# Optimization experiments

Measured on AMD Instinct MI355X. Metric: run time of the kernel, lower is better.

Reference implementation:

```python
import jax, jax.numpy as jnp
import numpy as np

INF = 10000.0

# ---------- differentiable (jax) pieces ----------

def _embed(x, W1, b1, W2, b2):
    # nn.Sequential(Linear, Dropout(eval=identity), ReLU, Linear, ReLU)
    h = jax.nn.relu(x @ W1.T + b1)
    return jax.nn.relu(h @ W2.T + b2)


def _cdist(a, b):
    # batched euclidean cdist with zero-safe sqrt (matches torch.cdist values)
    sq = (jnp.sum(a * a, -1)[:, :, None]
          + jnp.sum(b * b, -1)[:, None, :]
          - 2.0 * jnp.einsum('bnd,bmd->bnm', a, b))
    sq = jnp.maximum(sq, 0.0)
    safe = jnp.where(sq > 0, sq, 1.0)
    return jnp.where(sq > 0, jnp.sqrt(safe), 0.0)


def _edit_costs(x_s, x_t, W1, b1, W2, b2, virtual, B, N):
    D = W2.shape[0]
    es = _embed(x_s, W1, b1, W2, b2).reshape(B, N, D)
    et = _embed(x_t, W1, b1, W2, b2).reshape(B, N, D)
    v = _embed(virtual[None, :], W1, b1, W2, b2)          # [1, D]
    vb = jnp.broadcast_to(v[None, :, :], (B, 1, D))
    es = jnp.concatenate([es, vb], axis=1)                # [B, N+1, D]
    et = jnp.concatenate([et, vb], axis=1)
    d = _cdist(es, et)                                    # [B, N+1, N+1]
    # per-pair normalization: d / sum(d) * (len_s * len_t)
    d = d / jnp.sum(d, axis=(1, 2), keepdims=True) * float(N * N)
    return d

# ---------- host-side LSAPE (replaces scipy.optimize.linear_sum_assignment) ----------

def _lsap(C):
    # Jonker-Volgenant / shortest augmenting path, square cost matrix.
    n = C.shape[0]
    u = np.zeros(n + 1)
    v = np.zeros(n + 1)
    p = np.zeros(n + 1, np.int64)    # p[j] = row matched to column j (1-indexed)
    way = np.zeros(n + 1, np.int64)
    for i in range(1, n + 1):
        p[0] = i
        j0 = 0
        minv = np.full(n + 1, np.inf)
        used = np.zeros(n + 1, bool)
        while True:
            used[j0] = True
            i0 = p[j0]
            free = np.nonzero(~used)[0]
            cur = C[i0 - 1, free - 1] - u[i0] - v[free]
            better = cur < minv[free]
            minv[free] = np.where(better, cur, minv[free])
            way[free] = np.where(better, j0, way[free])
            k = int(np.argmin(minv[free]))
            j1 = int(free[k])
            delta = minv[free][k]
            u[p[used]] += delta
            v[used] -= delta
            minv[free] -= delta
            j0 = j1
            if p[j0] == 0:
                break
        while j0 != 0:
            j1 = int(way[j0])
            p[j0] = p[j1]
            j0 = j1
    rows = p[1:] - 1
    cols = np.arange(n)
    return rows, cols


def _lsape(ec, n, m):
    # ec: (n+1, m+1) edit costs with virtual row/col; build (n+m)x(n+m) LSAPE matrix
    C = np.zeros((n + m, n + m))
    C[:n, :m] = ec[:n, :m]
    C[n:, :m] = INF
    C[:n, m:] = INF
    C[np.arange(n, n + m), np.arange(m)] = ec[n, :m]       # insertions
    C[np.arange(n), np.arange(m, m + n)] = ec[:n, m]       # deletions
    C[~np.isfinite(C)] = INF
    q, p = _lsap(C)
    A = np.zeros((n + 1, m + 1), np.int64)
    A[np.minimum(q, n), np.minimum(p, m)] = 1
    A[-1, -1] = 0
    return A

# ---------- harness ----------

def setup_inputs() -> dict:
    B, N, FIN, D = 16, 128, 512, 512
    key = jax.random.key(0)
    ks = jax.random.split(key, 7)
    s1 = 1.0 / np.sqrt(FIN)
    s2 = 1.0 / np.sqrt(D)
    return {
        'x_s': jax.random.normal(ks[0], (B * N, FIN), jnp.float32),
        'x_t': jax.random.normal(ks[1], (B * N, FIN), jnp.float32),
        'W1': jax.random.uniform(ks[2], (D, FIN), jnp.float32, -s1, s1),
        'b1': jax.random.uniform(ks[3], (D,), jnp.float32, -s1, s1),
        'W2': jax.random.uniform(ks[4], (D, D), jnp.float32, -s2, s2),
        'b2': jax.random.uniform(ks[5], (D,), jnp.float32, -s2, s2),
        'virtual': jax.random.uniform(ks[6], (FIN,), jnp.float32),
        'npairs': 16,
        'n_nodes': 128,
    }


def reference(x_s, x_t, W1, b1, W2, b2, virtual, npairs, n_nodes):
    B, N = int(npairs), int(n_nodes)
    edit = _edit_costs(x_s, x_t, W1, b1, W2, b2, virtual, B, N)  # [B, N+1, N+1]
    ec_np = np.asarray(jax.device_get(edit), np.float64)
    aligns = np.stack([_lsape(ec_np[i], N, N) for i in range(B)])
    A = jnp.asarray(aligns)                                      # [B, N+1, N+1] int
    geds = jnp.sum(A * edit, axis=(1, 2)) / float(2 * N)         # / (len_s + len_t)
    return (A, edit, geds)
```

## Files before the change

### kernel.cpp

```cpp
#include <hip/hip_runtime.h>

#define BATCH 16
#define NNODE 128
#define DIM 512
#define NP1 129
#define EDSZ (NP1 * NP1)
#define BIGF 3.0e38f

__global__ __launch_bounds__(256) void gemm2_nt_relu(
    const float* __restrict__ X0, const float* __restrict__ X1,
    const float* __restrict__ VS,
    const float* __restrict__ W, const float* __restrict__ bias,
    float* __restrict__ Y0, float* __restrict__ Y1,
    int M, int N, int K) {
  if (blockIdx.x == gridDim.x - 1 && blockIdx.z) return;
  const float* X = blockIdx.z ? X1 : X0;
  float* Y = blockIdx.z ? Y1 : Y0;
  __shared__ float sA[32][68];
  __shared__ float sB[32][68];
  const int tid = threadIdx.x;
  const int m0 = blockIdx.x * 64;
  const int n0 = blockIdx.y * 64;
  const int tm = tid / 16, tn = tid % 16;
  const int lr = tid >> 2;
  const int lk8 = (tid & 3) * 8;
  const int row = m0 + lr;
  const float* xrow = (row < M) ? (X + (size_t)row * K) : VS;
  const float* wrow = W + (size_t)(n0 + lr) * K;
  float acc[4][4] = {};
  for (int k0 = 0; k0 < K; k0 += 32) {
    const float* xa = xrow + k0 + lk8;
    const float* wb = wrow + k0 + lk8;
    float4 a0 = *(const float4*)(xa);
    float4 a1 = *(const float4*)(xa + 4);
    float4 b0 = *(const float4*)(wb);
    float4 b1 = *(const float4*)(wb + 4);
    sA[lk8 + 0][lr] = a0.x; sA[lk8 + 1][lr] = a0.y;
    sA[lk8 + 2][lr] = a0.z; sA[lk8 + 3][lr] = a0.w;
    sA[lk8 + 4][lr] = a1.x; sA[lk8 + 5][lr] = a1.y;
    sA[lk8 + 6][lr] = a1.z; sA[lk8 + 7][lr] = a1.w;
    sB[lk8 + 0][lr] = b0.x; sB[lk8 + 1][lr] = b0.y;
    sB[lk8 + 2][lr] = b0.z; sB[lk8 + 3][lr] = b0.w;
    sB[lk8 + 4][lr] = b1.x; sB[lk8 + 5][lr] = b1.y;
    sB[lk8 + 6][lr] = b1.z; sB[lk8 + 7][lr] = b1.w;
    __syncthreads();
#pragma unroll
    for (int k = 0; k < 32; ++k) {
      const float4 a = *(const float4*)&sA[k][tm * 4];
      const float4 b = *(const float4*)&sB[k][tn * 4];
      acc[0][0] = fmaf(a.x, b.x, acc[0][0]);
      acc[0][1] = fmaf(a.x, b.y, acc[0][1]);
      acc[0][2] = fmaf(a.x, b.z, acc[0][2]);
      acc[0][3] = fmaf(a.x, b.w, acc[0][3]);
      acc[1][0] = fmaf(a.y, b.x, acc[1][0]);
      acc[1][1] = fmaf(a.y, b.y, acc[1][1]);
      acc[1][2] = fmaf(a.y, b.z, acc[1][2]);
      acc[1][3] = fmaf(a.y, b.w, acc[1][3]);
      acc[2][0] = fmaf(a.z, b.x, acc[2][0]);
      acc[2][1] = fmaf(a.z, b.y, acc[2][1]);
      acc[2][2] = fmaf(a.z, b.z, acc[2][2]);
      acc[2][3] = fmaf(a.z, b.w, acc[2][3]);
      acc[3][0] = fmaf(a.w, b.x, acc[3][0]);
      acc[3][1] = fmaf(a.w, b.y, acc[3][1]);
      acc[3][2] = fmaf(a.w, b.z, acc[3][2]);
      acc[3][3] = fmaf(a.w, b.w, acc[3][3]);
    }
    __syncthreads();
  }
#pragma unroll
  for (int i = 0; i < 4; ++i) {
    int m = m0 + tm * 4 + i;
#pragma unroll
    for (int j = 0; j < 4; ++j) {
      int n = n0 + tn * 4 + j;
      if (m <= M)
        Y[(size_t)m * N + n] = fmaxf(acc[i][j] + bias[n], 0.f);
    }
  }
}

__global__ __launch_bounds__(256) void cdist_kernel(
    const float* __restrict__ es, const float* __restrict__ et,
    const float* __restrict__ ev, float* __restrict__ d) {
  const int b = blockIdx.z;
  const int i0 = blockIdx.x * 32;
  const int j0 = blockIdx.y * 32;
  __shared__ float sA[32][33];
  __shared__ float sB[32][33];
  const int tid = threadIdx.x;
  const int ty = tid / 16, tx = tid % 16;
  const int lr = tid / 8;
  const int lk4 = (tid % 8) * 4;
  const int gi = i0 + lr;
  const int gj = j0 + lr;
  const float* pa = (gi < NNODE) ? (es + ((size_t)b * NNODE + gi) * DIM) : ev;
  const float* pb = (gj < NNODE) ? (et + ((size_t)b * NNODE + gj) * DIM) : ev;
  float acc[2][2] = {};
  for (int k0 = 0; k0 < DIM; k0 += 32) {
    float4 av = *(const float4*)(pa + k0 + lk4);
    float4 bv = *(const float4*)(pb + k0 + lk4);
    sA[lr][lk4 + 0] = av.x; sA[lr][lk4 + 1] = av.y;
    sA[lr][lk4 + 2] = av.z; sA[lr][lk4 + 3] = av.w;
    sB[lr][lk4 + 0] = bv.x; sB[lr][lk4 + 1] = bv.y;
    sB[lr][lk4 + 2] = bv.z; sB[lr][lk4 + 3] = bv.w;
    __syncthreads();
#pragma unroll 8
    for (int k = 0; k < 32; ++k) {
      float a0 = sA[ty * 2 + 0][k], a1 = sA[ty * 2 + 1][k];
      float b0 = sB[tx * 2 + 0][k], b1 = sB[tx * 2 + 1][k];
      float d00 = a0 - b0, d01 = a0 - b1, d10 = a1 - b0, d11 = a1 - b1;
      acc[0][0] = fmaf(d00, d00, acc[0][0]);
      acc[0][1] = fmaf(d01, d01, acc[0][1]);
      acc[1][0] = fmaf(d10, d10, acc[1][0]);
      acc[1][1] = fmaf(d11, d11, acc[1][1]);
    }
    __syncthreads();
  }
#pragma unroll
  for (int i = 0; i < 2; ++i) {
    int gi2 = i0 + ty * 2 + i;
#pragma unroll
    for (int j = 0; j < 2; ++j) {
      int gj2 = j0 + tx * 2 + j;
      if (gi2 < NP1 && gj2 < NP1)
        d[(size_t)b * EDSZ + gi2 * NP1 + gj2] = sqrtf(acc[i][j]);
    }
  }
}

__global__ __launch_bounds__(256) void sum_normalize(
    const float* __restrict__ d, float* __restrict__ edit) {
  const int b = blockIdx.x;
  const float* db = d + (size_t)b * EDSZ;
  float* eb = edit + (size_t)b * EDSZ;
  double s = 0.0;
  for (int idx = threadIdx.x; idx < EDSZ; idx += 256)
    s += (double)db[idx];
  __shared__ double red[256];
  red[threadIdx.x] = s;
  __syncthreads();
  for (int off = 128; off; off >>= 1) {
    if (threadIdx.x < off) red[threadIdx.x] += red[threadIdx.x + off];
    __syncthreads();
  }
  const float sum = (float)red[0];
  for (int idx = threadIdx.x; idx < EDSZ; idx += 256)
    eb[idx] = db[idx] / sum * (float)(NNODE * NNODE);
}

__device__ __forceinline__ unsigned key_of(float m, int col) {
  return (__float_as_uint(m) & 0xFFFFFF80u) | (unsigned)col;
}

__device__ __forceinline__ float readlane_f32(float x, int lane) {
  return __uint_as_float(
      (unsigned)__builtin_amdgcn_readlane((int)__float_as_uint(x), lane));
}

template <int CTRL>
__device__ __forceinline__ unsigned dpp_umin_step(unsigned x) {
  const unsigned o = (unsigned)__builtin_amdgcn_update_dpp(
      (int)0xFFFFFFFFu, (int)x, CTRL, 0xf, 0xf, false);
  return o < x ? o : x;
}

__device__ __forceinline__ unsigned wave_umin_key(unsigned x) {
  x = dpp_umin_step<0x111>(x);
  x = dpp_umin_step<0x112>(x);
  x = dpp_umin_step<0x114>(x);
  x = dpp_umin_step<0x118>(x);
  x = dpp_umin_step<0x142>(x);
  x = dpp_umin_step<0x143>(x);
  return (unsigned)__builtin_amdgcn_readlane((int)x, 63);
}

template <int CTRL>
__device__ __forceinline__ void dpp_umin2_step(unsigned& m1, unsigned& m2) {
  const unsigned o1 = (unsigned)__builtin_amdgcn_update_dpp(
      (int)0xFFFFFFFFu, (int)m1, CTRL, 0xf, 0xf, false);
  const unsigned o2 = (unsigned)__builtin_amdgcn_update_dpp(
      (int)0xFFFFFFFFu, (int)m2, CTRL, 0xf, 0xf, false);
  const unsigned lo = m1 < o1 ? m1 : o1;
  const unsigned hi = m1 < o1 ? o1 : m1;
  const unsigned yo = m2 < o2 ? m2 : o2;
  m1 = lo;
  m2 = hi < yo ? hi : yo;
}

__device__ __forceinline__ void wave_umin2_key(unsigned a, unsigned b,
                                               unsigned& k1, unsigned& k2) {
  unsigned m1 = a < b ? a : b;
  unsigned m2 = a < b ? b : a;
  dpp_umin2_step<0x111>(m1, m2);
  dpp_umin2_step<0x112>(m1, m2);
  dpp_umin2_step<0x114>(m1, m2);
  dpp_umin2_step<0x118>(m1, m2);
  dpp_umin2_step<0x142>(m1, m2);
  dpp_umin2_step<0x143>(m1, m2);
  k1 = (unsigned)__builtin_amdgcn_readlane((int)m1, 63);
  k2 = (unsigned)__builtin_amdgcn_readlane((int)m2, 63);
}

__device__ __forceinline__ float bcast_pair_f(float a0, float a1, int idx) {
  const int l = idx >> 1;
  const float xa = readlane_f32(a0, l);
  const float xb = readlane_f32(a1, l);
  return (idx & 1) ? xb : xa;
}
__device__ __forceinline__ int bcast_pair_i(int a0, int a1, int idx) {
  const int l = idx >> 1;
  const int xa = __builtin_amdgcn_readlane(a0, l);
  const int xb = __builtin_amdgcn_readlane(a1, l);
  return (idx & 1) ? xb : xa;
}

__global__ __launch_bounds__(64) void lsap_kernel(
    const float* __restrict__ edit, float* __restrict__ Aout,
    float* __restrict__ geds) {
  const int b = blockIdx.x;
  const float* ec = edit + (size_t)b * EDSZ;
  float* A = Aout + (size_t)b * EDSZ;
  const int lane = threadIdx.x;
  const int cbase = lane * 2;

  __shared__ float D[NNODE * NNODE];

  for (int idx = lane; idx < NNODE * NNODE; idx += 64) {
    const int i = idx >> 7, j = idx & 127;
    const float sub = ec[i * NP1 + j];
    const float di = ec[i * NP1 + NNODE] + ec[NNODE * NP1 + j];
    D[idx] = fminf(sub, di);
  }
  __syncthreads();

  const float* Dl = D + cbase;

  float u0 = 0.f, u1 = 0.f;
  float v0 = 0.f, v1 = 0.f;
  float m0, m1;
  int w0 = 0, w1 = 0;
  int p0 = 0, p1 = 0;
  int x0 = 0, x1 = 0;

  int y0 = 0, y1 = 0;
  {
    float c0 = BIGF, c1 = BIGF;
    for (int r = 0; r < NNODE; ++r) {
      const float2 f = *(const float2*)(Dl + (r << 7));
      if (f.x < c0) { c0 = f.x; y0 = r; }
      if (f.y < c1) { c1 = f.y; y1 = r; }
    }
    v0 = c0; v1 = c1;
  }

  unsigned long long ra0 = 0, ra1 = 0;
  for (int j = 0; j < NNODE; ++j) {
    const int i1 = bcast_pair_i(y0, y1, j);
    const int bit = i1 & 63;
    const unsigned long long msk = (i1 < 64) ? ra0 : ra1;
    if (!((msk >> bit) & 1ull)) {
      if (i1 < 64) ra0 |= 1ull << bit; else ra1 |= 1ull << bit;
      const bool oj = lane == (j >> 1);
      p0 = (oj && !(j & 1)) ? i1 + 1 : p0;
      p1 = (oj &&  (j & 1)) ? i1 + 1 : p1;
      const bool oi = lane == (i1 >> 1);
      x0 = (oi && !(i1 & 1)) ? j + 1 : x0;
      x1 = (oi &&  (i1 & 1)) ? j + 1 : x1;
    }
  }

  for (int ii = 0; ii < NNODE; ++ii) {
    const float2 f = *(const float2*)(Dl + (ii << 7));
    const int xj = bcast_pair_i(x0, x1, ii);
    if (xj == 0) continue;
    const int j1 = xj - 1;
    float r0 = fmaxf(f.x - v0, 0.f);
    float r1 = fmaxf(f.y - v1, 0.f);
    if (cbase + 0 == j1) r0 = BIGF;
    if (cbase + 1 == j1) r1 = BIGF;
    const unsigned ka = key_of(r0, cbase + 0);
    const unsigned kb = key_of(r1, cbase + 1);
    const unsigned kmin = wave_umin_key(ka < kb ? ka : kb);
    const int jm = (int)(kmin & 127u);
    const float umin = bcast_pair_f(r0, r1, jm);
    const bool ov = lane == (j1 >> 1);
    v0 = (ov && !(j1 & 1)) ? v0 - umin : v0;
    v1 = (ov &&  (j1 & 1)) ? v1 - umin : v1;
    const bool ou = lane == (ii >> 1);
    u0 = (ou && !(ii & 1)) ? umin : u0;
    u1 = (ou &&  (ii & 1)) ? umin : u1;
  }

  {
    int nfree_prev =
        NNODE - __builtin_popcountll(ra0) - __builtin_popcountll(ra1);
    for (int pass = 0; pass < 8 && nfree_prev; ++pass) {
      unsigned long long todo0 = ~ra0, todo1 = ~ra1;
      while (todo0 | todo1) {
        int i;
        if (todo0) { i = __builtin_ctzll(todo0); todo0 &= todo0 - 1ull; }
        else       { i = 64 + __builtin_ctzll(todo1); todo1 &= todo1 - 1ull; }

        const float2 f = *(const float2*)(Dl + (i << 7));
        const float r0 = fmaxf(f.x - v0, 0.f);
        const float r1 = fmaxf(f.y - v1, 0.f);
        unsigned k1, k2;
        wave_umin2_key(key_of(r0, cbase + 0), key_of(r1, cbase + 1), k1, k2);
        const int j1 = (int)(k1 & 127u), j2 = (int)(k2 & 127u);
        const float u1v = bcast_pair_f(r0, r1, j1);
        const float u2v = bcast_pair_f(r0, r1, j2);

        int jt = j1;
        int i1 = bcast_pair_i(p0, p1, j1);
        if (u1v < u2v) {
          const float dv = u2v - u1v;
          const bool ov = lane == (j1 >> 1);
          v0 = (ov && !(j1 & 1)) ? v0 - dv : v0;
          v1 = (ov &&  (j1 & 1)) ? v1 - dv : v1;
        } else if (i1 != 0) {
          jt = j2;
          i1 = bcast_pair_i(p0, p1, j2);
        }
        {
          const bool oj = lane == (jt >> 1);
          p0 = (oj && !(jt & 1)) ? i + 1 : p0;
          p1 = (oj &&  (jt & 1)) ? i + 1 : p1;
          const bool oi = lane == (i >> 1);
          u0 = (oi && !(i & 1)) ? u2v : u0;
          u1 = (oi &&  (i & 1)) ? u2v : u1;
        }
        if (i < 64) ra0 |= 1ull << i; else ra1 |= 1ull << (i - 64);
        if (i1 != 0) {
          const int rr = i1 - 1;
          if (rr < 64) ra0 &= ~(1ull << rr); else ra1 &= ~(1ull << (rr - 64));
        }
      }
      const int nfree_now =
          NNODE - __builtin_popcountll(ra0) - __builtin_popcountll(ra1);
      if (nfree_now == nfree_prev) break;
      nfree_prev = nfree_now;
    }
  }

  for (int ii = 0; ii < NNODE; ++ii) {
    const unsigned long long amsk = (ii < 64) ? ra0 : ra1;
    if ((amsk >> (ii & 63)) & 1ull) continue;
    const int i = ii + 1;

    unsigned cused = 0, rused = 0;
    m0 = m1 = BIGF;
    int j0 = 0;
    int i0 = i;
    for (int guard = 0; guard <= NNODE; ++guard) {
      const float2 f = *(const float2*)(Dl + ((i0 - 1) << 7));

      const float u_i0 = bcast_pair_f(u0, u1, i0 - 1);

      {
        const int jm1 = j0 - 1;
        const bool oc = (j0 > 0) && (lane == (jm1 >> 1));
        const bool c0m = oc && !(jm1 & 1);
        const bool c1m = oc &&  (jm1 & 1);
        cused |= c0m ? 1u : 0u;
        cused |= c1m ? 2u : 0u;
        m0 = c0m ? BIGF : m0;
        m1 = c1m ? BIGF : m1;
        const int im1 = i0 - 1;
        const bool orow = lane == (im1 >> 1);
        rused |= (orow && !(im1 & 1)) ? 1u : 0u;
        rused |= (orow &&  (im1 & 1)) ? 2u : 0u;
      }

      {
        const float cur0 = fmaxf(f.x - u_i0 - v0, 0.f);
        const bool up0 = !(cused & 1u) && (cur0 < m0);
        m0 = up0 ? cur0 : m0;
        w0 = up0 ? j0 : w0;
        const float cur1 = fmaxf(f.y - u_i0 - v1, 0.f);
        const bool up1 = !(cused & 2u) && (cur1 < m1);
        m1 = up1 ? cur1 : m1;
        w1 = up1 ? j0 : w1;
      }

      const unsigned ka = key_of(m0, cbase + 0);
      const unsigned kb = key_of(m1, cbase + 1);
      const unsigned kmin = wave_umin_key(ka < kb ? ka : kb);
      const int jcol = (int)(kmin & 127u);
      const float delta = bcast_pair_f(m0, m1, jcol);
      const int pj1 = bcast_pair_i(p0, p1, jcol);

      {
        const bool used0 = (cused & 1u) != 0;
        const bool used1 = (cused & 2u) != 0;
        v0 = used0 ? v0 - delta : v0;
        v1 = used1 ? v1 - delta : v1;
        m0 = used0 ? m0 : fmaxf(m0 - delta, 0.f);
        m1 = used1 ? m1 : fmaxf(m1 - delta, 0.f);
        u0 = (rused & 1u) ? u0 + delta : u0;
        u1 = (rused & 2u) ? u1 + delta : u1;
      }

      j0 = jcol + 1;
      if (pj1 == 0) break;
      i0 = pj1;
    }

    int jc = j0;
    while (jc != 0) {
      const int jp = bcast_pair_i(w0, w1, jc - 1);
      const int js = (jp == 0) ? 1 : jp;
      const int pvr = bcast_pair_i(p0, p1, js - 1);
      const int pv = (jp == 0) ? i : pvr;
      const bool oc = lane == ((jc - 1) >> 1);
      p0 = (oc && !((jc - 1) & 1)) ? pv : p0;
      p1 = (oc &&  ((jc - 1) & 1)) ? pv : p1;
      jc = jp;
    }
  }

  double contrib = 0.0;
  {
    const int pr[2] = {p0, p1};
#pragma unroll
    for (int q = 0; q < 2; ++q) {
      const int j = cbase + q;
      const int i = pr[q] - 1;
      const float sub = ec[i * NP1 + j];
      const float di = ec[i * NP1 + NNODE] + ec[NNODE * NP1 + j];
      if (sub < di) {
        A[i * NP1 + j] = 1.f;
        contrib += (double)sub;
      } else {
        A[i * NP1 + NNODE] = 1.f;
        A[NNODE * NP1 + j] = 1.f;
        contrib += (double)di;
      }
    }
  }
#pragma unroll
  for (int off = 32; off; off >>= 1) contrib += __shfl_xor(contrib, off);
  if (lane == 0) geds[b] = (float)(contrib / 256.0);
}

extern "C" void kernel_launch(void* const* d_in, const int* in_sizes, int n_in,
                              void* d_out, int out_size, void* d_ws, size_t ws_size,
                              hipStream_t stream) {
  const float* x_s  = (const float*)d_in[0];
  const float* x_t  = (const float*)d_in[1];
  const float* W1   = (const float*)d_in[2];
  const float* b1   = (const float*)d_in[3];
  const float* W2   = (const float*)d_in[4];
  const float* b2   = (const float*)d_in[5];
  const float* virt = (const float*)d_in[6];

  const int M = BATCH * NNODE;

  float* ws    = (float*)d_ws;
  float* h_s   = ws;
  float* h_t   = h_s + ((size_t)M + 1) * DIM;
  float* e_s   = h_t + (size_t)M * DIM;
  float* e_t   = e_s + ((size_t)M + 1) * DIM;
  float* d_raw = e_t + (size_t)M * DIM;

  float* Aout = (float*)d_out;
  float* edit = Aout + (size_t)BATCH * EDSZ;
  float* geds = edit + (size_t)BATCH * EDSZ;

  hipMemsetAsync(Aout, 0, (size_t)BATCH * EDSZ * sizeof(float), stream);

  dim3 gblk(M / 64 + 1, DIM / 64, 2);
  gemm2_nt_relu<<<gblk, 256, 0, stream>>>(x_s, x_t, virt, W1, b1,
                                          h_s, h_t, M, DIM, DIM);
  gemm2_nt_relu<<<gblk, 256, 0, stream>>>(h_s, h_t, h_s + (size_t)M * DIM,
                                          W2, b2, e_s, e_t, M, DIM, DIM);

  const float* e_v = e_s + (size_t)M * DIM;
  cdist_kernel<<<dim3(5, 5, BATCH), 256, 0, stream>>>(e_s, e_t, e_v, d_raw);
  sum_normalize<<<BATCH, 256, 0, stream>>>(d_raw, edit);
  lsap_kernel<<<BATCH, 64, 0, stream>>>(edit, Aout, geds);
}
```

Measured before the change: 718.2 us.

## Fuse sum/normalize into cdist atomics and LSAP; drop memset and DPP row steps

Removes the separate sum_normalize kernel. cdist now reduces per-wave partial sums and atomically adds them into per-batch double accumulators, which are zeroed by the first GEMM. The LSAP kernel applies the normalization itself and zeroes the A output, replacing the memset. The wave min reduction swaps its last two DPP broadcast steps for four readlanes and a scalar min. This saves two launches and a pass over memory, but the single-wave LSAP blocks now do extra serial normalization work and the double atomics make the sum order nondeterministic.

```diff
diff --git a/kernel.cpp b/kernel.cpp
--- a/kernel.cpp
+++ b/kernel.cpp
@@ -12,8 +12,12 @@
     const float* __restrict__ VS,
     const float* __restrict__ W, const float* __restrict__ bias,
     float* __restrict__ Y0, float* __restrict__ Y1,
+    double* sums0,
     int M, int N, int K) {
   if (blockIdx.x == gridDim.x - 1 && blockIdx.z) return;
+  if (sums0 && blockIdx.x == 0 && blockIdx.y == 0 && blockIdx.z == 0 &&
+      threadIdx.x < BATCH)
+    sums0[threadIdx.x] = 0.0;
   const float* X = blockIdx.z ? X1 : X0;
   float* Y = blockIdx.z ? Y1 : Y0;
   __shared__ float sA[32][68];
@@ -81,7 +85,8 @@
 
 __global__ __launch_bounds__(256) void cdist_kernel(
     const float* __restrict__ es, const float* __restrict__ et,
-    const float* __restrict__ ev, float* __restrict__ d) {
+    const float* __restrict__ ev, float* __restrict__ d,
+    double* __restrict__ sums_d) {
   const int b = blockIdx.z;
   const int i0 = blockIdx.x * 32;
   const int j0 = blockIdx.y * 32;
@@ -116,36 +121,23 @@
     }
     __syncthreads();
   }
+  double psum = 0.0;
 #pragma unroll
   for (int i = 0; i < 2; ++i) {
     int gi2 = i0 + ty * 2 + i;
 #pragma unroll
     for (int j = 0; j < 2; ++j) {
       int gj2 = j0 + tx * 2 + j;
-      if (gi2 < NP1 && gj2 < NP1)
-        d[(size_t)b * EDSZ + gi2 * NP1 + gj2] = sqrtf(acc[i][j]);
-    }
-  }
-}
-
-__global__ __launch_bounds__(256) void sum_normalize(
-    const float* __restrict__ d, float* __restrict__ edit) {
-  const int b = blockIdx.x;
-  const float* db = d + (size_t)b * EDSZ;
-  float* eb = edit + (size_t)b * EDSZ;
-  double s = 0.0;
-  for (int idx = threadIdx.x; idx < EDSZ; idx += 256)
-    s += (double)db[idx];
-  __shared__ double red[256];
-  red[threadIdx.x] = s;
-  __syncthreads();
-  for (int off = 128; off; off >>= 1) {
-    if (threadIdx.x < off) red[threadIdx.x] += red[threadIdx.x + off];
-    __syncthreads();
-  }
-  const float sum = (float)red[0];
-  for (int idx = threadIdx.x; idx < EDSZ; idx += 256)
-    eb[idx] = db[idx] / sum * (float)(NNODE * NNODE);
+      if (gi2 < NP1 && gj2 < NP1) {
+        const float s = sqrtf(acc[i][j]);
+        d[(size_t)b * EDSZ + gi2 * NP1 + gj2] = s;
+        psum += (double)s;
+      }
+    }
+  }
+#pragma unroll
+  for (int off = 32; off; off >>= 1) psum += __shfl_xor(psum, off);
+  if ((tid & 63) == 0) atomicAdd(&sums_d[b], psum);
 }
 
 __device__ __forceinline__ unsigned key_of(float m, int col) {
@@ -169,9 +161,13 @@
   x = dpp_umin_step<0x112>(x);
   x = dpp_umin_step<0x114>(x);
   x = dpp_umin_step<0x118>(x);
-  x = dpp_umin_step<0x142>(x);
-  x = dpp_umin_step<0x143>(x);
-  return (unsigned)__builtin_amdgcn_readlane((int)x, 63);
+  const unsigned q0 = (unsigned)__builtin_amdgcn_readlane((int)x, 15);
+  const unsigned q1 = (unsigned)__builtin_amdgcn_readlane((int)x, 31);
+  const unsigned q2 = (unsigned)__builtin_amdgcn_readlane((int)x, 47);
+  const unsigned q3 = (unsigned)__builtin_amdgcn_readlane((int)x, 63);
+  const unsigned m01 = q0 < q1 ? q0 : q1;
+  const unsigned m23 = q2 < q3 ? q2 : q3;
+  return m01 < m23 ? m01 : m23;
 }
 
 template <int CTRL>
@@ -215,20 +211,31 @@
 }
 
 __global__ __launch_bounds__(64) void lsap_kernel(
-    const float* __restrict__ edit, float* __restrict__ Aout,
+    const float* __restrict__ d_raw, const double* __restrict__ sums_d,
+    float* __restrict__ edit, float* __restrict__ Aout,
     float* __restrict__ geds) {
   const int b = blockIdx.x;
-  const float* ec = edit + (size_t)b * EDSZ;
+  const float* dr = d_raw + (size_t)b * EDSZ;
+  float* eb = edit + (size_t)b * EDSZ;
   float* A = Aout + (size_t)b * EDSZ;
   const int lane = threadIdx.x;
   const int cbase = lane * 2;
 
+  const float sumf = (float)sums_d[b];
+  const float nn = (float)(NNODE * NNODE);
+
+  for (int idx = lane; idx < EDSZ; idx += 64) {
+    eb[idx] = dr[idx] / sumf * nn;
+    A[idx] = 0.f;
+  }
+
   __shared__ float D[NNODE * NNODE];
 
   for (int idx = lane; idx < NNODE * NNODE; idx += 64) {
     const int i = idx >> 7, j = idx & 127;
-    const float sub = ec[i * NP1 + j];
-    const float di = ec[i * NP1 + NNODE] + ec[NNODE * NP1 + j];
+    const float sub = dr[i * NP1 + j] / sumf * nn;
+    const float di = dr[i * NP1 + NNODE] / sumf * nn +
+                     dr[NNODE * NP1 + j] / sumf * nn;
     D[idx] = fminf(sub, di);
   }
   __syncthreads();
@@ -425,8 +432,9 @@
     for (int q = 0; q < 2; ++q) {
       const int j = cbase + q;
       const int i = pr[q] - 1;
-      const float sub = ec[i * NP1 + j];
-      const float di = ec[i * NP1 + NNODE] + ec[NNODE * NP1 + j];
+      const float sub = dr[i * NP1 + j] / sumf * nn;
+      const float di = dr[i * NP1 + NNODE] / sumf * nn +
+                       dr[NNODE * NP1 + j] / sumf * nn;
       if (sub < di) {
         A[i * NP1 + j] = 1.f;
         contrib += (double)sub;
@@ -461,21 +469,21 @@
   float* e_s   = h_t + (size_t)M * DIM;
   float* e_t   = e_s + ((size_t)M + 1) * DIM;
   float* d_raw = e_t + (size_t)M * DIM;
+  double* sums_d = (double*)(d_raw + (size_t)BATCH * EDSZ);
 
   float* Aout = (float*)d_out;
   float* edit = Aout + (size_t)BATCH * EDSZ;
   float* geds = edit + (size_t)BATCH * EDSZ;
 
-  hipMemsetAsync(Aout, 0, (size_t)BATCH * EDSZ * sizeof(float), stream);
-
   dim3 gblk(M / 64 + 1, DIM / 64, 2);
   gemm2_nt_relu<<<gblk, 256, 0, stream>>>(x_s, x_t, virt, W1, b1,
-                                          h_s, h_t, M, DIM, DIM);
+                                          h_s, h_t, sums_d, M, DIM, DIM);
   gemm2_nt_relu<<<gblk, 256, 0, stream>>>(h_s, h_t, h_s + (size_t)M * DIM,
-                                          W2, b2, e_s, e_t, M, DIM, DIM);
+                                          W2, b2, e_s, e_t, nullptr,
+                                          M, DIM, DIM);
 
   const float* e_v = e_s + (size_t)M * DIM;
-  cdist_kernel<<<dim3(5, 5, BATCH), 256, 0, stream>>>(e_s, e_t, e_v, d_raw);
-  sum_normalize<<<BATCH, 256, 0, stream>>>(d_raw, edit);
-  lsap_kernel<<<BATCH, 64, 0, stream>>>(edit, Aout, geds);
-}
+  cdist_kernel<<<dim3(5, 5, BATCH), 256, 0, stream>>>(e_s, e_t, e_v, d_raw,
+                                                      sums_d);
+  lsap_kernel<<<BATCH, 64, 0, stream>>>(d_raw, sums_d, edit, Aout, geds);
+}
```

Result: slower. 733.6 us (+2.1%).
